# Optimization experiments

Hardware: AMD Instinct MI355X
Metric: run time of the kernel (lower is better)

Reference implementation:

```python
import jax, jax.numpy as jnp
import numpy as np

C = 256
LN_EPS = 1e-5
LEAKY_SLOPE = 0.01

def _layernorm(t, g, b):
    mu = jnp.mean(t, axis=-1, keepdims=True)
    var = jnp.mean((t - mu) ** 2, axis=-1, keepdims=True)
    return (t - mu) * jax.lax.rsqrt(var + LN_EPS) * g + b

def setup_inputs() -> dict:
    key = jax.random.key(0)
    ks = jax.random.split(key, 16)
    b, d, h, w = 4, 4096, 64, 64
    s = lambda n: 1.0 / np.sqrt(n)
    return {
        "x": jax.random.normal(ks[0], (b, 1, d), jnp.float32),
        "y": jax.random.normal(ks[1], (b, C, h, w), jnp.float32),
        "q_w": jax.random.normal(ks[2], (C, C), jnp.float32) * s(C),
        "q_b": jnp.zeros((C,), jnp.float32),
        "dw_w": jax.random.normal(ks[3], (C,), jnp.float32),
        "dw_b": jnp.zeros((C,), jnp.float32),
        "kv_w1": jax.random.normal(ks[4], (1, C // 2), jnp.float32),
        "kv_b1": jnp.zeros((C // 2,), jnp.float32),
        "ln1_g": jnp.ones((C // 2,), jnp.float32),
        "ln1_b": jnp.zeros((C // 2,), jnp.float32),
        "kv_w2": jax.random.normal(ks[5], (C // 2, C), jnp.float32) * s(C // 2),
        "kv_b2": jnp.zeros((C,), jnp.float32),
        "ln2_g": jnp.ones((C,), jnp.float32),
        "ln2_b": jnp.zeros((C,), jnp.float32),
        "kv_w3": jax.random.normal(ks[6], (C, C), jnp.float32) * s(C),
        "kv_b3": jnp.zeros((C,), jnp.float32),
        "ln3_g": jnp.ones((C,), jnp.float32),
        "ln3_b": jnp.zeros((C,), jnp.float32),
        "kv_w4": jax.random.normal(ks[7], (C, 2 * C), jnp.float32) * s(C),
        "kv_b4": jnp.zeros((2 * C,), jnp.float32),
        "proj_w": jax.random.normal(ks[8], (C, C), jnp.float32) * s(C),
        "proj_b": jnp.zeros((C,), jnp.float32),
    }

def reference(x, y, q_w, q_b, dw_w, dw_b, kv_w1, kv_b1, ln1_g, ln1_b,
              kv_w2, kv_b2, ln2_g, ln2_b, kv_w3, kv_b3, ln3_g, ln3_b,
              kv_w4, kv_b4, proj_w, proj_b):
    b, c, h, w = y.shape
    # x: [b, 1, d] -> [b, d, 1]; MLP kv-generator lifts each scalar to 2c channels
    t = jnp.swapaxes(x, 1, 2)  # [b, d, 1]
    t = jax.nn.leaky_relu(_layernorm(t @ kv_w1 + kv_b1, ln1_g, ln1_b), LEAKY_SLOPE)
    t = jax.nn.leaky_relu(_layernorm(t @ kv_w2 + kv_b2, ln2_g, ln2_b), LEAKY_SLOPE)
    t = jax.nn.leaky_relu(_layernorm(t @ kv_w3 + kv_b3, ln3_g, ln3_b), LEAKY_SLOPE)
    t = jax.nn.silu(t @ kv_w4 + kv_b4)  # [b, d, 2c]
    k, v = jnp.split(t, 2, axis=-1)  # each [b, d, c]
    k = jnp.swapaxes(k, 1, 2)  # [b, c, d]
    # q = dwconv1x1(conv1x1(y)): 1x1 conv is a channel matmul; depthwise 1x1 is per-channel affine
    q = jnp.einsum('bchw,oc->bohw', y, q_w) + q_b[None, :, None, None]
    q = q * dw_w[None, :, None, None] + dw_b[None, :, None, None]
    q = q.reshape(b, c, h * w).transpose(0, 2, 1)  # [b, hw, c]
    scores = jnp.einsum('bic,bcd->bid', q, k) * (float(c) ** -0.5)  # [b, hw, d]
    attn = jax.nn.softmax(scores, axis=2)
    h_ = jnp.einsum('bid,bdc->bic', attn, v)  # [b, hw, c]
    h_ = h_.transpose(0, 2, 1).reshape(b, c, h, w)
    h_ = jnp.einsum('bchw,oc->bohw', h_, proj_w) + proj_b[None, :, None, None]
    return y + h_
```

## Files before the change

kernel.cpp:

```cpp
#include <hip/hip_runtime.h>
#include <cstdint>
#include <cstddef>

using bf16   = __bf16;
using bf16x8 = __bf16 __attribute__((ext_vector_type(8)));
using f32x4  = float  __attribute__((ext_vector_type(4)));
using u16    = unsigned short;
using ushort8 = __attribute__((ext_vector_type(8))) unsigned short;

#define MFMA16(a, b, c) __builtin_amdgcn_mfma_f32_16x16x32_bf16(a, b, c, 0, 0, 0)

__device__ __forceinline__ u16 f2bf(float f) {
  union { float f; unsigned u; } v; v.f = f;
  unsigned r = v.u + 0x7fffu + ((v.u >> 16) & 1u);
  return (u16)(r >> 16);
}
__device__ __forceinline__ u16 bfc(float f) {
  union { float f; unsigned u; } v; v.f = f;
  return (u16)((v.u + 0x8000u) >> 16);
}
__device__ __forceinline__ float b2f(u16 h) {
  union { unsigned u; float f; } v; v.u = ((unsigned)h) << 16; return v.f;
}
__device__ __forceinline__ bf16x8 ldb8(const u16* p) { return *(const bf16x8*)p; }
__device__ __forceinline__ float red_sum16(float v) {
  v += __shfl_xor(v, 1, 64); v += __shfl_xor(v, 2, 64);
  v += __shfl_xor(v, 4, 64); v += __shfl_xor(v, 8, 64);
  return v;
}
__device__ __forceinline__ void gll16(const u16* g, u16* l) {
  __builtin_amdgcn_global_load_lds(
      (const __attribute__((address_space(1))) void*)g,
      (__attribute__((address_space(3))) void*)l, 16, 0, 0);
}

#define QSCALE 0.09016844005556021f

__global__ __launch_bounds__(256) void k_prep_mlp1(
    const float* __restrict__ kv_w2, const float* __restrict__ kv_w3,
    const float* __restrict__ kv_w4, const float* __restrict__ q_w,
    const float* __restrict__ proj_w,
    u16* __restrict__ Wt2, u16* __restrict__ Wt3, u16* __restrict__ Wt4,
    u16* __restrict__ Qw, u16* __restrict__ Pww,
    const float* __restrict__ x, const float* __restrict__ w1,
    const float* __restrict__ b1, const float* __restrict__ g, const float* __restrict__ bb,
    u16* __restrict__ T1) {
  if (blockIdx.x >= 4096) {
    int idx = (blockIdx.x - 4096) * 256 + threadIdx.x;
    if (idx < 32768) {
      int n = idx >> 7, k = idx & 127;
      Wt2[idx] = f2bf(kv_w2[k * 256 + n]);
    } else if (idx < 98304) {
      int j = idx - 32768, n = j >> 8, k = j & 255;
      Wt3[j] = f2bf(kv_w3[k * 256 + n]);
    } else if (idx < 229376) {
      int j = idx - 98304, n = j >> 8, k = j & 255;
      Wt4[j] = f2bf(kv_w4[k * 512 + n]);
    } else if (idx < 294912) {
      int j = idx - 229376;
      Qw[j] = f2bf(q_w[j]);
    } else if (idx < 360448) {
      int j = idx - 294912;
      Pww[j] = f2bf(proj_w[j]);
    }
    return;
  }
  int lane = threadIdx.x & 63;
  int r = blockIdx.x * 4 + (threadIdx.x >> 6);
  float xv = x[r];
  float t0 = xv * w1[lane] + b1[lane];
  float t1 = xv * w1[lane + 64] + b1[lane + 64];
  float s = t0 + t1;
  #pragma unroll
  for (int m = 1; m <= 32; m <<= 1) s += __shfl_xor(s, m, 64);
  float mu = s * (1.f / 128.f);
  float d0 = t0 - mu, d1 = t1 - mu;
  float vv = d0 * d0 + d1 * d1;
  #pragma unroll
  for (int m = 1; m <= 32; m <<= 1) vv += __shfl_xor(vv, m, 64);
  float inv = rsqrtf(vv * (1.f / 128.f) + 1e-5f);
  float o0 = d0 * inv * g[lane] + bb[lane];
  float o1 = d1 * inv * g[lane + 64] + bb[lane + 64];
  o0 = o0 > 0.f ? o0 : 0.01f * o0;
  o1 = o1 > 0.f ? o1 : 0.01f * o1;
  T1[(size_t)r * 128 + lane]      = f2bf(o0);
  T1[(size_t)r * 128 + lane + 64] = f2bf(o1);
}

template<int K, int NC>
__global__ __launch_bounds__(128) void k_gemm_ln(const u16* __restrict__ A, const u16* __restrict__ Bt,
    const float* __restrict__ bias, const float* __restrict__ g, const float* __restrict__ bb,
    u16* __restrict__ out) {
  constexpr int LD = K + 8;
  constexpr int CPR = K / 8;
  __shared__ u16 sA[32 * LD];
  __shared__ u16 sB[NC * LD];
  int tid = threadIdx.x, w = tid >> 6, lane = tid & 63, quad = lane >> 4, l16 = lane & 15;
  int i0 = blockIdx.x * 32;
  #pragma unroll
  for (int p = 0; p < (32 * CPR) / 128; ++p) {
    int q = p * 128 + tid; int row = q / CPR, c8 = q - row * CPR;
    *(uint4*)(sA + row * LD + c8 * 8) = *(const uint4*)(A + (size_t)(i0 + row) * K + c8 * 8);
  }
  f32x4 z = {0.f, 0.f, 0.f, 0.f};
  f32x4 acc[16];
  #pragma unroll
  for (int f = 0; f < 16; ++f) acc[f] = z;
  bf16x8 af[K / 32];
  constexpr int NCH = 256 / NC;
  for (int nc = 0; nc < NCH; ++nc) {
    if (nc) __syncthreads();
    #pragma unroll
    for (int p = 0; p < (NC * CPR) / 128; ++p) {
      int q = p * 128 + tid; int row = q / CPR, c8 = q - row * CPR;
      *(uint4*)(sB + row * LD + c8 * 8) = *(const uint4*)(Bt + (size_t)(nc * NC + row) * K + c8 * 8);
    }
    __syncthreads();
    if (nc == 0) {
      #pragma unroll
      for (int kk = 0; kk < K / 32; ++kk) af[kk] = ldb8(sA + (w * 16 + l16) * LD + kk * 32 + quad * 8);
    }
    #pragma unroll
    for (int nb = 0; nb < NC / 16; ++nb) {
      int f = nc * (NC / 16) + nb;
      #pragma unroll
      for (int kk = 0; kk < K / 32; ++kk) {
        bf16x8 bfr = ldb8(sB + (nb * 16 + l16) * LD + kk * 32 + quad * 8);
        acc[f] = MFMA16(af[kk], bfr, acc[f]);
      }
    }
  }
  #pragma unroll
  for (int f = 0; f < 16; ++f) {
    float bv = bias[f * 16 + l16];
    acc[f][0] += bv; acc[f][1] += bv; acc[f][2] += bv; acc[f][3] += bv;
  }
  #pragma unroll
  for (int r = 0; r < 4; ++r) {
    float s = 0;
    #pragma unroll
    for (int f = 0; f < 16; ++f) s += acc[f][r];
    s = red_sum16(s);
    float mu = s * (1.f / 256.f);
    float vv = 0;
    #pragma unroll
    for (int f = 0; f < 16; ++f) { float d = acc[f][r] - mu; vv += d * d; }
    vv = red_sum16(vv);
    float inv = rsqrtf(vv * (1.f / 256.f) + 1e-5f);
    int rowg = i0 + w * 16 + quad * 4 + r;
    #pragma unroll
    for (int f = 0; f < 16; ++f) {
      int col = f * 16 + l16;
      float o = (acc[f][r] - mu) * inv * g[col] + bb[col];
      o = o > 0.f ? o : 0.01f * o;
      out[(size_t)rowg * 256 + col] = f2bf(o);
    }
  }
}

__global__ __launch_bounds__(256) void k_gemm_silu(const u16* __restrict__ A, const u16* __restrict__ Bt,
    const float* __restrict__ bias, u16* __restrict__ Kt, u16* __restrict__ Vt) {
  constexpr int LD = 264, NC = 32;
  __shared__ u16 sA[64 * LD];
  __shared__ u16 sB[NC * LD];
  int tid = threadIdx.x, w = tid >> 6, lane = tid & 63, quad = lane >> 4, l16 = lane & 15;
  int i0 = blockIdx.x * 64;
  int half = blockIdx.y;
  #pragma unroll
  for (int p = 0; p < 8; ++p) {
    int q = p * 256 + tid; int row = q >> 5, c8 = q & 31;
    *(uint4*)(sA + row * LD + c8 * 8) = *(const uint4*)(A + (size_t)(i0 + row) * 256 + c8 * 8);
  }
  f32x4 z = {0.f, 0.f, 0.f, 0.f};
  f32x4 acc[16];
  #pragma unroll
  for (int f = 0; f < 16; ++f) acc[f] = z;
  bf16x8 af[8];
  for (int nc = 0; nc < 8; ++nc) {
    if (nc) __syncthreads();
    #pragma unroll
    for (int p = 0; p < 4; ++p) {
      int q = p * 256 + tid; int row = q >> 5, c8 = q & 31;
      *(uint4*)(sB + row * LD + c8 * 8) =
          *(const uint4*)(Bt + (size_t)(half * 256 + nc * NC + row) * 256 + c8 * 8);
    }
    __syncthreads();
    if (nc == 0) {
      #pragma unroll
      for (int kk = 0; kk < 8; ++kk) af[kk] = ldb8(sA + (w * 16 + l16) * LD + kk * 32 + quad * 8);
    }
    #pragma unroll
    for (int nb = 0; nb < 2; ++nb) {
      int f = nc * 2 + nb;
      #pragma unroll
      for (int kk = 0; kk < 8; ++kk) {
        bf16x8 bfr = ldb8(sB + (nb * 16 + l16) * LD + kk * 32 + quad * 8);
        acc[f] = MFMA16(af[kk], bfr, acc[f]);
      }
    }
  }
  #pragma unroll
  for (int f = 0; f < 16; ++f) {
    int col = f * 16 + l16;
    float bv = bias[half * 256 + col];
    if (half == 0) {
      int chunk = f * 2 + (l16 >> 3), co = col & 7;
      #pragma unroll
      for (int r = 0; r < 4; ++r) {
        int rowg = i0 + w * 16 + quad * 4 + r;
        float v = acc[f][r] + bv;
        v = v / (1.f + __expf(-v));
        int chs = (chunk + (rowg & 31)) & 31;
        Kt[(size_t)rowg * 256 + chs * 8 + co] = f2bf(v);
      }
    } else {
      int rowg0 = i0 + w * 16 + quad * 4;
      int bb2 = rowg0 >> 12, d0 = rowg0 & 4095;
      int dd = d0 & 31, qd = dd >> 3;
      int chs = (qd + (col & 3) + ((col >> 2) & 3)) & 3;
      ushort4 u;
      #pragma unroll
      for (int r = 0; r < 4; ++r) {
        float v = acc[f][r] + bv;
        v = v / (1.f + __expf(-v));
        ((u16*)&u)[r] = f2bf(v);
      }
      size_t off = ((size_t)(bb2 * 128 + (d0 >> 5)) * 8192) + col * 32 + chs * 8 + (dd & 7);
      *(ushort4*)(Vt + off) = u;
    }
  }
}

__global__ __launch_bounds__(128) void k_gemm_q(const float* __restrict__ y, const u16* __restrict__ Qw,
    const float* __restrict__ qb, const float* __restrict__ dww, const float* __restrict__ dwb,
    u16* __restrict__ Qb) {
  __shared__ u16 sY[32 * 72];
  __shared__ u16 sB[256 * 72];
  int tid = threadIdx.x, w = tid >> 6, lane = tid & 63, quad = lane >> 4, l16 = lane & 15;
  int b = blockIdx.x >> 7, i0 = (blockIdx.x & 127) * 32;
  f32x4 z = {0.f, 0.f, 0.f, 0.f};
  f32x4 acc[16];
  #pragma unroll
  for (int f = 0; f < 16; ++f) acc[f] = z;
  for (int kc = 0; kc < 4; ++kc) {
    if (kc) __syncthreads();
    {
      int cl = tid >> 3;
      int il = (tid & 7) * 4;
      #pragma unroll
      for (int p = 0; p < 4; ++p) {
        int c = kc * 64 + p * 16 + cl;
        float4 v = *(const float4*)(y + ((size_t)(b * 256 + c)) * 4096 + i0 + il);
        sY[(il + 0) * 72 + p * 16 + cl] = f2bf(v.x);
        sY[(il + 1) * 72 + p * 16 + cl] = f2bf(v.y);
        sY[(il + 2) * 72 + p * 16 + cl] = f2bf(v.z);
        sY[(il + 3) * 72 + p * 16 + cl] = f2bf(v.w);
      }
    }
    #pragma unroll
    for (int p = 0; p < 16; ++p) {
      int q = p * 128 + tid; int row = q >> 3, k8 = q & 7;
      *(uint4*)(sB + row * 72 + k8 * 8) = *(const uint4*)(Qw + (size_t)row * 256 + kc * 64 + k8 * 8);
    }
    __syncthreads();
    #pragma unroll
    for (int kk = 0; kk < 2; ++kk) {
      bf16x8 af = ldb8(sY + (w * 16 + l16) * 72 + kk * 32 + quad * 8);
      #pragma unroll
      for (int f = 0; f < 16; ++f) {
        bf16x8 bfr = ldb8(sB + (f * 16 + l16) * 72 + kk * 32 + quad * 8);
        acc[f] = MFMA16(af, bfr, acc[f]);
      }
    }
  }
  #pragma unroll
  for (int f = 0; f < 16; ++f) {
    int col = f * 16 + l16;
    float q0 = qb[col], sc = dww[col], dB = dwb[col];
    #pragma unroll
    for (int r = 0; r < 4; ++r) {
      int rowg = i0 + w * 16 + quad * 4 + r;
      float v = ((acc[f][r] + q0) * sc + dB) * QSCALE;
      Qb[((size_t)(b * 4096 + rowg)) * 256 + col] = f2bf(v);
    }
  }
}

__global__ __launch_bounds__(256, 2) void k_attn(const u16* __restrict__ Qb, const u16* __restrict__ Kt,
    const u16* __restrict__ Vt, u16* __restrict__ Op, float* __restrict__ Ol) {
  __shared__ __align__(16) u16 smem[37888];
  int tid = threadIdx.x, w = tid >> 6, lane = tid & 63, quad = lane >> 4, l16 = lane & 15;
  int b = blockIdx.x & 3, kh = (blockIdx.x >> 2) & 3, qt = blockIdx.x >> 4;
  int i0 = qt * 128 + w * 32;

  bf16x8 qf[2][8];
  {
    const u16* qrow = Qb + ((size_t)(b * 4096 + i0 + l16)) * 256 + quad * 8;
    #pragma unroll
    for (int kk = 0; kk < 8; ++kk) {
      qf[0][kk] = ldb8(qrow + kk * 32);
      qf[1][kk] = ldb8(qrow + 16 * 256 + kk * 32);
    }
  }
  f32x4 z = {0.f, 0.f, 0.f, 0.f};
  f32x4 oacc[2][16];
  #pragma unroll
  for (int sub = 0; sub < 2; ++sub)
    #pragma unroll
    for (int f = 0; f < 16; ++f) oacc[sub][f] = z;
  float l4[2][4] = {{0.f, 0.f, 0.f, 0.f}, {0.f, 0.f, 0.f, 0.f}};

  u16* sPw = smem + 32768 + w * 1280;
  int wp = w & 1;
  const u16* gSrc = ((w < 2) ? Kt : Vt) + ((size_t)(b * 128 + kh * 32) * 8192) + wp * 4096 + lane * 8;
  u16* lBase = smem + ((w < 2) ? 0 : 8192) + wp * 4096 + lane * 8;

  #pragma unroll
  for (int i = 0; i < 8; ++i) gll16(gSrc + i * 512, lBase + i * 512);
  gSrc += 8192;

  #pragma unroll 1
  for (int kt = 0; kt < 32; ++kt) {
    int buf = kt & 1;
    const u16* sK = smem + buf * 16384;
    const u16* sV = sK + 8192;
    asm volatile("s_waitcnt vmcnt(0)" ::: "memory");
    __syncthreads();
    if (kt < 31) {
      u16* dst = lBase + (buf ^ 1) * 16384;
      #pragma unroll
      for (int i = 0; i < 8; ++i) gll16(gSrc + i * 512, dst + i * 512);
      gSrc += 8192;
    }
    f32x4 s00 = z, s01 = z, s10 = z, s11 = z;
    #pragma unroll
    for (int kk = 0; kk < 8; ++kk) {
      int ch0 = (kk * 4 + quad + l16) & 31;
      int ch1 = (ch0 + 16) & 31;
      bf16x8 k0 = ldb8(sK + l16 * 256 + ch0 * 8);
      bf16x8 k1 = ldb8(sK + (16 + l16) * 256 + ch1 * 8);
      s00 = MFMA16(qf[0][kk], k0, s00);
      s01 = MFMA16(qf[0][kk], k1, s01);
      s10 = MFMA16(qf[1][kk], k0, s10);
      s11 = MFMA16(qf[1][kk], k1, s11);
    }
    #pragma unroll
    for (int r = 0; r < 4; ++r) {
      float p0 = exp2f(s00[r]);
      float p1 = exp2f(s01[r]);
      float p2 = exp2f(s10[r]);
      float p3 = exp2f(s11[r]);
      l4[0][r] += p0 + p1;
      l4[1][r] += p2 + p3;
      int row0 = (quad * 4 + r) * 40;
      sPw[row0 + l16]            = bfc(p0);
      sPw[row0 + 16 + l16]       = bfc(p1);
      sPw[640 + row0 + l16]      = bfc(p2);
      sPw[640 + row0 + 16 + l16] = bfc(p3);
    }
    asm volatile("s_waitcnt lgkmcnt(0)" ::: "memory");
    bf16x8 pf0 = ldb8(sPw + l16 * 40 + quad * 8);
    bf16x8 pf1 = ldb8(sPw + 640 + l16 * 40 + quad * 8);
    #pragma unroll
    for (int f = 0; f < 16; ++f) {
      int c = f * 16 + l16;
      int chs = (quad + (c & 3) + ((c >> 2) & 3)) & 3;
      bf16x8 vf = ldb8(sV + c * 32 + chs * 8);
      oacc[0][f] = MFMA16(pf0, vf, oacc[0][f]);
      oacc[1][f] = MFMA16(pf1, vf, oacc[1][f]);
    }
  }
  #pragma unroll
  for (int sub = 0; sub < 2; ++sub)
    #pragma unroll
    for (int r = 0; r < 4; ++r) l4[sub][r] = red_sum16(l4[sub][r]);
  #pragma unroll
  for (int sub = 0; sub < 2; ++sub)
    #pragma unroll
    for (int r = 0; r < 4; ++r) {
      size_t gr = (size_t)kh * 16384 + b * 4096 + i0 + sub * 16 + quad * 4 + r;
      u16* orow = Op + gr * 256;
      #pragma unroll
      for (int f = 0; f < 16; ++f) orow[f * 16 + l16] = f2bf(oacc[sub][f][r]);
      if (l16 == 0) Ol[gr] = l4[sub][r];
    }
}

__global__ __launch_bounds__(256) void k_proj(const u16* __restrict__ Op, const float* __restrict__ Ol,
    const u16* __restrict__ Pw, const float* __restrict__ pb, const float* __restrict__ y,
    float* __restrict__ out) {
  __shared__ u16 sA[64 * 136];
  __shared__ u16 sB[64 * 136];
  __shared__ float sW[64];
  int tid = threadIdx.x, w = tid >> 6, lane = tid & 63, quad = lane >> 4, l16 = lane & 15;
  int i0 = blockIdx.x * 64, o0 = blockIdx.y * 64, b = blockIdx.z;
  if (tid < 64) {
    size_t gr = (size_t)b * 4096 + i0 + tid;
    float L = Ol[gr] + Ol[gr + 16384] + Ol[gr + 32768] + Ol[gr + 49152];
    sW[tid] = 1.f / L;
  }
  __syncthreads();
  f32x4 z = {0.f, 0.f, 0.f, 0.f};
  f32x4 acc[4] = {z, z, z, z};
  for (int kc = 0; kc < 2; ++kc) {
    if (kc) __syncthreads();
    #pragma unroll
    for (int p = 0; p < 4; ++p) {
      int q = p * 256 + tid; int row = q >> 4, c8 = q & 15;
      *(uint4*)(sA + row * 136 + c8 * 8) = *(const uint4*)(Pw + ((size_t)(o0 + row)) * 256 + kc * 128 + c8 * 8);
      size_t gr = (size_t)b * 4096 + i0 + row;
      const u16* hp = Op + gr * 256 + kc * 128 + c8 * 8;
      uint4 u0 = *(const uint4*)(hp);
      uint4 u1 = *(const uint4*)(hp + 4194304);
      uint4 u2 = *(const uint4*)(hp + 8388608);
      uint4 u3 = *(const uint4*)(hp + 12582912);
      float wr = sW[row];
      const u16* p0 = (const u16*)&u0; const u16* p1 = (const u16*)&u1;
      const u16* p2 = (const u16*)&u2; const u16* p3 = (const u16*)&u3;
      ushort8 ov;
      #pragma unroll
      for (int e = 0; e < 8; ++e) {
        float v = (b2f(p0[e]) + b2f(p1[e]) + b2f(p2[e]) + b2f(p3[e])) * wr;
        ov[e] = f2bf(v);
      }
      *(ushort8*)(sB + row * 136 + c8 * 8) = ov;
    }
    __syncthreads();
    #pragma unroll
    for (int kk = 0; kk < 4; ++kk) {
      bf16x8 af = ldb8(sA + (w * 16 + l16) * 136 + kk * 32 + quad * 8);
      #pragma unroll
      for (int nb = 0; nb < 4; ++nb) {
        bf16x8 bfr = ldb8(sB + (nb * 16 + l16) * 136 + kk * 32 + quad * 8);
        acc[nb] = MFMA16(af, bfr, acc[nb]);
      }
    }
  }
  #pragma unroll
  for (int nb = 0; nb < 4; ++nb) {
    #pragma unroll
    for (int r = 0; r < 4; ++r) {
      int og = o0 + w * 16 + quad * 4 + r;
      size_t idx = ((size_t)(b * 256 + og)) * 4096 + i0 + nb * 16 + l16;
      out[idx] = y[idx] + acc[nb][r] + pb[og];
    }
  }
}

extern "C" void kernel_launch(void* const* d_in, const int* in_sizes, int n_in,
                              void* d_out, int out_size, void* d_ws, size_t ws_size,
                              hipStream_t stream) {
  (void)in_sizes; (void)n_in; (void)out_size; (void)ws_size;
  const float* x     = (const float*)d_in[0];
  const float* y     = (const float*)d_in[1];
  const float* q_w   = (const float*)d_in[2];
  const float* q_b   = (const float*)d_in[3];
  const float* dw_w  = (const float*)d_in[4];
  const float* dw_b  = (const float*)d_in[5];
  const float* kv_w1 = (const float*)d_in[6];
  const float* kv_b1 = (const float*)d_in[7];
  const float* ln1_g = (const float*)d_in[8];
  const float* ln1_b = (const float*)d_in[9];
  const float* kv_w2 = (const float*)d_in[10];
  const float* kv_b2 = (const float*)d_in[11];
  const float* ln2_g = (const float*)d_in[12];
  const float* ln2_b = (const float*)d_in[13];
  const float* kv_w3 = (const float*)d_in[14];
  const float* kv_b3 = (const float*)d_in[15];
  const float* ln3_g = (const float*)d_in[16];
  const float* ln3_b = (const float*)d_in[17];
  const float* kv_w4 = (const float*)d_in[18];
  const float* kv_b4 = (const float*)d_in[19];
  const float* proj_w = (const float*)d_in[20];
  const float* proj_b = (const float*)d_in[21];
  float* out = (float*)d_out;
  unsigned char* ws = (unsigned char*)d_ws;

  u16* Wt2 = (u16*)(ws + 0);
  u16* Wt3 = (u16*)(ws + 65536);
  u16* Wt4 = (u16*)(ws + 196608);
  u16* Qw  = (u16*)(ws + 458752);
  u16* Pww = (u16*)(ws + 589824);
  u16* T2  = (u16*)(ws + 1048576);
  u16* T3  = (u16*)(ws + 9437184);
  u16* Qb  = T3;
  u16* Kt  = (u16*)(ws + 17825792);
  u16* T1  = Kt;
  u16* Vt  = (u16*)(ws + 26214400);
  u16* Op  = (u16*)(ws + 34603008);
  float* Ol = (float*)(ws + 68157440);

  k_prep_mlp1<<<5504, 256, 0, stream>>>(kv_w2, kv_w3, kv_w4, q_w, proj_w,
                                        Wt2, Wt3, Wt4, Qw, Pww,
                                        x, kv_w1, kv_b1, ln1_g, ln1_b, T1);
  k_gemm_ln<128, 64><<<512, 128, 0, stream>>>(T1, Wt2, kv_b2, ln2_g, ln2_b, T2);
  k_gemm_ln<256, 32><<<512, 128, 0, stream>>>(T2, Wt3, kv_b3, ln3_g, ln3_b, T3);
  k_gemm_silu<<<dim3(256, 2), 256, 0, stream>>>(T3, Wt4, kv_b4, Kt, Vt);
  k_gemm_q<<<512, 128, 0, stream>>>(y, Qw, q_b, dw_w, dw_b, Qb);
  k_attn<<<512, 256, 0, stream>>>(Qb, Kt, Vt, Op, Ol);
  k_proj<<<dim3(64, 4, 4), 256, 0, stream>>>(Op, Ol, Pww, proj_b, y, out);
}
```

Measured before the change: 269.5 us.

## Fuse the kv MLP layers and Q projection into one kernel

The first LayerNorm, the three kv-MLP GEMM+LN layers and the SiLU output layer are merged into one kernel that keeps each 64-row activation tile in shared memory. This removes the intermediate T1/T2/T3 global round trips and several launches. The Q projection runs as extra blocks of the same launch so it can overlap with the MLP blocks. The cost is a larger shared-memory footprint per block and more serialized work per block, with fewer blocks available for the MLP.

Measured after the change: 269.1 us. About the same (-0.1%).

```diff
diff --git a/kernel.cpp b/kernel.cpp
--- a/kernel.cpp
+++ b/kernel.cpp
@@ -36,100 +36,33 @@
 
 #define QSCALE 0.09016844005556021f
 
-__global__ __launch_bounds__(256) void k_prep_mlp1(
-    const float* __restrict__ kv_w2, const float* __restrict__ kv_w3,
-    const float* __restrict__ kv_w4, const float* __restrict__ q_w,
-    const float* __restrict__ proj_w,
-    u16* __restrict__ Wt2, u16* __restrict__ Wt3, u16* __restrict__ Wt4,
-    u16* __restrict__ Qw, u16* __restrict__ Pww,
-    const float* __restrict__ x, const float* __restrict__ w1,
-    const float* __restrict__ b1, const float* __restrict__ g, const float* __restrict__ bb,
-    u16* __restrict__ T1) {
-  if (blockIdx.x >= 4096) {
-    int idx = (blockIdx.x - 4096) * 256 + threadIdx.x;
-    if (idx < 32768) {
-      int n = idx >> 7, k = idx & 127;
-      Wt2[idx] = f2bf(kv_w2[k * 256 + n]);
-    } else if (idx < 98304) {
-      int j = idx - 32768, n = j >> 8, k = j & 255;
-      Wt3[j] = f2bf(kv_w3[k * 256 + n]);
-    } else if (idx < 229376) {
-      int j = idx - 98304, n = j >> 8, k = j & 255;
-      Wt4[j] = f2bf(kv_w4[k * 512 + n]);
-    } else if (idx < 294912) {
-      int j = idx - 229376;
-      Qw[j] = f2bf(q_w[j]);
-    } else if (idx < 360448) {
-      int j = idx - 294912;
-      Pww[j] = f2bf(proj_w[j]);
-    }
-    return;
-  }
-  int lane = threadIdx.x & 63;
-  int r = blockIdx.x * 4 + (threadIdx.x >> 6);
-  float xv = x[r];
-  float t0 = xv * w1[lane] + b1[lane];
-  float t1 = xv * w1[lane + 64] + b1[lane + 64];
-  float s = t0 + t1;
-  #pragma unroll
-  for (int m = 1; m <= 32; m <<= 1) s += __shfl_xor(s, m, 64);
-  float mu = s * (1.f / 128.f);
-  float d0 = t0 - mu, d1 = t1 - mu;
-  float vv = d0 * d0 + d1 * d1;
-  #pragma unroll
-  for (int m = 1; m <= 32; m <<= 1) vv += __shfl_xor(vv, m, 64);
-  float inv = rsqrtf(vv * (1.f / 128.f) + 1e-5f);
-  float o0 = d0 * inv * g[lane] + bb[lane];
-  float o1 = d1 * inv * g[lane + 64] + bb[lane + 64];
-  o0 = o0 > 0.f ? o0 : 0.01f * o0;
-  o1 = o1 > 0.f ? o1 : 0.01f * o1;
-  T1[(size_t)r * 128 + lane]      = f2bf(o0);
-  T1[(size_t)r * 128 + lane + 64] = f2bf(o1);
-}
-
-template<int K, int NC>
-__global__ __launch_bounds__(128) void k_gemm_ln(const u16* __restrict__ A, const u16* __restrict__ Bt,
-    const float* __restrict__ bias, const float* __restrict__ g, const float* __restrict__ bb,
-    u16* __restrict__ out) {
-  constexpr int LD = K + 8;
-  constexpr int CPR = K / 8;
-  __shared__ u16 sA[32 * LD];
-  __shared__ u16 sB[NC * LD];
-  int tid = threadIdx.x, w = tid >> 6, lane = tid & 63, quad = lane >> 4, l16 = lane & 15;
-  int i0 = blockIdx.x * 32;
-  #pragma unroll
-  for (int p = 0; p < (32 * CPR) / 128; ++p) {
-    int q = p * 128 + tid; int row = q / CPR, c8 = q - row * CPR;
-    *(uint4*)(sA + row * LD + c8 * 8) = *(const uint4*)(A + (size_t)(i0 + row) * K + c8 * 8);
-  }
-  f32x4 z = {0.f, 0.f, 0.f, 0.f};
-  f32x4 acc[16];
-  #pragma unroll
-  for (int f = 0; f < 16; ++f) acc[f] = z;
-  bf16x8 af[K / 32];
-  constexpr int NCH = 256 / NC;
-  for (int nc = 0; nc < NCH; ++nc) {
-    if (nc) __syncthreads();
-    #pragma unroll
-    for (int p = 0; p < (NC * CPR) / 128; ++p) {
-      int q = p * 128 + tid; int row = q / CPR, c8 = q - row * CPR;
-      *(uint4*)(sB + row * LD + c8 * 8) = *(const uint4*)(Bt + (size_t)(nc * NC + row) * K + c8 * 8);
-    }
-    __syncthreads();
-    if (nc == 0) {
-      #pragma unroll
-      for (int kk = 0; kk < K / 32; ++kk) af[kk] = ldb8(sA + (w * 16 + l16) * LD + kk * 32 + quad * 8);
-    }
-    #pragma unroll
-    for (int nb = 0; nb < NC / 16; ++nb) {
-      int f = nc * (NC / 16) + nb;
-      #pragma unroll
-      for (int kk = 0; kk < K / 32; ++kk) {
-        bf16x8 bfr = ldb8(sB + (nb * 16 + l16) * LD + kk * 32 + quad * 8);
-        acc[f] = MFMA16(af[kk], bfr, acc[f]);
-      }
-    }
-  }
+__global__ void k_prep(const float* __restrict__ kv_w2, const float* __restrict__ kv_w3,
+                       const float* __restrict__ kv_w4, const float* __restrict__ q_w,
+                       const float* __restrict__ proj_w,
+                       u16* __restrict__ Wt2, u16* __restrict__ Wt3, u16* __restrict__ Wt4,
+                       u16* __restrict__ Qw, u16* __restrict__ Pww) {
+  int idx = blockIdx.x * 256 + threadIdx.x;
+  if (idx < 32768) {
+    int n = idx >> 7, k = idx & 127;
+    Wt2[idx] = f2bf(kv_w2[k * 256 + n]);
+  } else if (idx < 98304) {
+    int j = idx - 32768, n = j >> 8, k = j & 255;
+    Wt3[j] = f2bf(kv_w3[k * 256 + n]);
+  } else if (idx < 229376) {
+    int j = idx - 98304, n = j >> 8, k = j & 255;
+    Wt4[j] = f2bf(kv_w4[k * 512 + n]);
+  } else if (idx < 294912) {
+    int j = idx - 229376;
+    Qw[j] = f2bf(q_w[j]);
+  } else if (idx < 360448) {
+    int j = idx - 294912;
+    Pww[j] = f2bf(proj_w[j]);
+  }
+}
+
+__device__ __forceinline__ void ln_store(f32x4* acc, const float* __restrict__ bias,
+    const float* __restrict__ g, const float* __restrict__ bb, u16* act,
+    int w, int quad, int l16) {
   #pragma unroll
   for (int f = 0; f < 16; ++f) {
     float bv = bias[f * 16 + l16];
@@ -147,97 +80,166 @@
     for (int f = 0; f < 16; ++f) { float d = acc[f][r] - mu; vv += d * d; }
     vv = red_sum16(vv);
     float inv = rsqrtf(vv * (1.f / 256.f) + 1e-5f);
-    int rowg = i0 + w * 16 + quad * 4 + r;
+    int rl = w * 16 + quad * 4 + r;
     #pragma unroll
     for (int f = 0; f < 16; ++f) {
       int col = f * 16 + l16;
       float o = (acc[f][r] - mu) * inv * g[col] + bb[col];
       o = o > 0.f ? o : 0.01f * o;
-      out[(size_t)rowg * 256 + col] = f2bf(o);
-    }
-  }
-}
-
-__global__ __launch_bounds__(256) void k_gemm_silu(const u16* __restrict__ A, const u16* __restrict__ Bt,
-    const float* __restrict__ bias, u16* __restrict__ Kt, u16* __restrict__ Vt) {
-  constexpr int LD = 264, NC = 32;
-  __shared__ u16 sA[64 * LD];
-  __shared__ u16 sB[NC * LD];
-  int tid = threadIdx.x, w = tid >> 6, lane = tid & 63, quad = lane >> 4, l16 = lane & 15;
-  int i0 = blockIdx.x * 64;
-  int half = blockIdx.y;
-  #pragma unroll
-  for (int p = 0; p < 8; ++p) {
-    int q = p * 256 + tid; int row = q >> 5, c8 = q & 31;
-    *(uint4*)(sA + row * LD + c8 * 8) = *(const uint4*)(A + (size_t)(i0 + row) * 256 + c8 * 8);
-  }
+      act[rl * 264 + col] = f2bf(o);
+    }
+  }
+}
+
+template<int K>
+__device__ __forceinline__ void mlp_layer(u16* act, u16* sW, const u16* __restrict__ Wt,
+    const float* __restrict__ bias, const float* __restrict__ g, const float* __restrict__ bb,
+    int tid, int w, int quad, int l16) {
+  bf16x8 af[K / 32];
+  #pragma unroll
+  for (int kk = 0; kk < K / 32; ++kk) af[kk] = ldb8(act + (w * 16 + l16) * 264 + kk * 32 + quad * 8);
   f32x4 z = {0.f, 0.f, 0.f, 0.f};
   f32x4 acc[16];
   #pragma unroll
   for (int f = 0; f < 16; ++f) acc[f] = z;
-  bf16x8 af[8];
   for (int nc = 0; nc < 8; ++nc) {
-    if (nc) __syncthreads();
-    #pragma unroll
-    for (int p = 0; p < 4; ++p) {
-      int q = p * 256 + tid; int row = q >> 5, c8 = q & 31;
-      *(uint4*)(sB + row * LD + c8 * 8) =
-          *(const uint4*)(Bt + (size_t)(half * 256 + nc * NC + row) * 256 + c8 * 8);
-    }
     __syncthreads();
-    if (nc == 0) {
-      #pragma unroll
-      for (int kk = 0; kk < 8; ++kk) af[kk] = ldb8(sA + (w * 16 + l16) * LD + kk * 32 + quad * 8);
-    }
+    #pragma unroll
+    for (int p = 0; p < K / 64; ++p) {
+      int q = p * 256 + tid; int row = q / (K / 8), c8 = q % (K / 8);
+      *(uint4*)(sW + row * 264 + c8 * 8) = *(const uint4*)(Wt + (size_t)(nc * 32 + row) * K + c8 * 8);
+    }
+    __syncthreads();
     #pragma unroll
     for (int nb = 0; nb < 2; ++nb) {
       int f = nc * 2 + nb;
       #pragma unroll
-      for (int kk = 0; kk < 8; ++kk) {
-        bf16x8 bfr = ldb8(sB + (nb * 16 + l16) * LD + kk * 32 + quad * 8);
-        acc[f] = MFMA16(af[kk], bfr, acc[f]);
-      }
-    }
-  }
-  #pragma unroll
-  for (int f = 0; f < 16; ++f) {
-    int col = f * 16 + l16;
-    float bv = bias[half * 256 + col];
-    if (half == 0) {
-      int chunk = f * 2 + (l16 >> 3), co = col & 7;
-      #pragma unroll
-      for (int r = 0; r < 4; ++r) {
-        int rowg = i0 + w * 16 + quad * 4 + r;
-        float v = acc[f][r] + bv;
-        v = v / (1.f + __expf(-v));
-        int chs = (chunk + (rowg & 31)) & 31;
-        Kt[(size_t)rowg * 256 + chs * 8 + co] = f2bf(v);
-      }
-    } else {
-      int rowg0 = i0 + w * 16 + quad * 4;
-      int bb2 = rowg0 >> 12, d0 = rowg0 & 4095;
-      int dd = d0 & 31, qd = dd >> 3;
-      int chs = (qd + (col & 3) + ((col >> 2) & 3)) & 3;
-      ushort4 u;
-      #pragma unroll
-      for (int r = 0; r < 4; ++r) {
-        float v = acc[f][r] + bv;
-        v = v / (1.f + __expf(-v));
-        ((u16*)&u)[r] = f2bf(v);
-      }
-      size_t off = ((size_t)(bb2 * 128 + (d0 >> 5)) * 8192) + col * 32 + chs * 8 + (dd & 7);
-      *(ushort4*)(Vt + off) = u;
-    }
-  }
-}
-
-__global__ __launch_bounds__(128) void k_gemm_q(const float* __restrict__ y, const u16* __restrict__ Qw,
+      for (int kk = 0; kk < K / 32; ++kk)
+        acc[f] = MFMA16(af[kk], ldb8(sW + (nb * 16 + l16) * 264 + kk * 32 + quad * 8), acc[f]);
+    }
+  }
+  ln_store(acc, bias, g, bb, act, w, quad, l16);
+  __syncthreads();
+}
+
+__device__ __forceinline__ void mlp_layer4(u16* act, u16* sW, const u16* __restrict__ Wt4,
+    const float* __restrict__ bias4, u16* __restrict__ Kt, u16* __restrict__ Vt,
+    int i0, int tid, int w, int quad, int l16) {
+  bf16x8 af[8];
+  #pragma unroll
+  for (int kk = 0; kk < 8; ++kk) af[kk] = ldb8(act + (w * 16 + l16) * 264 + kk * 32 + quad * 8);
+  f32x4 z = {0.f, 0.f, 0.f, 0.f};
+  for (int h = 0; h < 2; ++h) {
+    f32x4 acc[16];
+    #pragma unroll
+    for (int f = 0; f < 16; ++f) acc[f] = z;
+    for (int nc = 0; nc < 8; ++nc) {
+      __syncthreads();
+      #pragma unroll
+      for (int p = 0; p < 4; ++p) {
+        int q = p * 256 + tid; int row = q >> 5, c8 = q & 31;
+        *(uint4*)(sW + row * 264 + c8 * 8) =
+            *(const uint4*)(Wt4 + (size_t)(h * 256 + nc * 32 + row) * 256 + c8 * 8);
+      }
+      __syncthreads();
+      #pragma unroll
+      for (int nb = 0; nb < 2; ++nb) {
+        int f = nc * 2 + nb;
+        #pragma unroll
+        for (int kk = 0; kk < 8; ++kk)
+          acc[f] = MFMA16(af[kk], ldb8(sW + (nb * 16 + l16) * 264 + kk * 32 + quad * 8), acc[f]);
+      }
+    }
+    #pragma unroll
+    for (int f = 0; f < 16; ++f) {
+      int col = f * 16 + l16;
+      float bv = bias4[h * 256 + col];
+      if (h == 0) {
+        int chunk = f * 2 + (l16 >> 3), co = col & 7;
+        #pragma unroll
+        for (int r = 0; r < 4; ++r) {
+          int rowg = i0 + w * 16 + quad * 4 + r;
+          float v = acc[f][r] + bv;
+          v = v / (1.f + __expf(-v));
+          int chs = (chunk + (rowg & 31)) & 31;
+          Kt[(size_t)rowg * 256 + chs * 8 + co] = f2bf(v);
+        }
+      } else {
+        int rowg0 = i0 + w * 16 + quad * 4;
+        int bb2 = rowg0 >> 12, d0 = rowg0 & 4095;
+        int dd = d0 & 31, qd = dd >> 3;
+        int chs = (qd + (col & 3) + ((col >> 2) & 3)) & 3;
+        ushort4 u;
+        #pragma unroll
+        for (int r = 0; r < 4; ++r) {
+          float v = acc[f][r] + bv;
+          v = v / (1.f + __expf(-v));
+          ((u16*)&u)[r] = f2bf(v);
+        }
+        size_t off = ((size_t)(bb2 * 128 + (d0 >> 5)) * 8192) + col * 32 + chs * 8 + (dd & 7);
+        *(ushort4*)(Vt + off) = u;
+      }
+    }
+  }
+}
+
+__global__ __launch_bounds__(256, 2) void k_fused(
+    const float* __restrict__ x, const float* __restrict__ w1, const float* __restrict__ bias1,
+    const float* __restrict__ g1, const float* __restrict__ bb1,
+    const u16* __restrict__ Wt2, const float* __restrict__ bias2,
+    const float* __restrict__ g2, const float* __restrict__ bb2,
+    const u16* __restrict__ Wt3, const float* __restrict__ bias3,
+    const float* __restrict__ g3, const float* __restrict__ bb3,
+    const u16* __restrict__ Wt4, const float* __restrict__ bias4,
+    const float* __restrict__ y, const u16* __restrict__ Qw,
     const float* __restrict__ qb, const float* __restrict__ dww, const float* __restrict__ dwb,
-    u16* __restrict__ Qb) {
-  __shared__ u16 sY[32 * 72];
-  __shared__ u16 sB[256 * 72];
+    u16* __restrict__ Kt, u16* __restrict__ Vt, u16* __restrict__ Qb) {
+  __shared__ __align__(16) u16 smem[25344];
   int tid = threadIdx.x, w = tid >> 6, lane = tid & 63, quad = lane >> 4, l16 = lane & 15;
-  int b = blockIdx.x >> 7, i0 = (blockIdx.x & 127) * 32;
+
+  if (blockIdx.x < 256) {
+    u16* act = smem;
+    u16* sW  = smem + 16896;
+    int i0 = blockIdx.x * 64;
+    {
+      int rloc = w * 16 + (lane >> 2);
+      int c0 = (lane & 3) * 32;
+      float xv = x[i0 + rloc];
+      float t[32];
+      float s = 0.f;
+      #pragma unroll
+      for (int j = 0; j < 32; ++j) { t[j] = xv * w1[c0 + j] + bias1[c0 + j]; s += t[j]; }
+      s += __shfl_xor(s, 1, 64); s += __shfl_xor(s, 2, 64);
+      float mu = s * (1.f / 128.f);
+      float vv = 0.f;
+      #pragma unroll
+      for (int j = 0; j < 32; ++j) { float d = t[j] - mu; vv += d * d; }
+      vv += __shfl_xor(vv, 1, 64); vv += __shfl_xor(vv, 2, 64);
+      float inv = rsqrtf(vv * (1.f / 128.f) + 1e-5f);
+      #pragma unroll
+      for (int jo = 0; jo < 4; ++jo) {
+        ushort8 pk;
+        #pragma unroll
+        for (int e = 0; e < 8; ++e) {
+          int j = jo * 8 + e;
+          float o = (t[j] - mu) * inv * g1[c0 + j] + bb1[c0 + j];
+          o = o > 0.f ? o : 0.01f * o;
+          pk[e] = f2bf(o);
+        }
+        *(ushort8*)(act + rloc * 264 + c0 + jo * 8) = pk;
+      }
+    }
+    __syncthreads();
+    mlp_layer<128>(act, sW, Wt2, bias2, g2, bb2, tid, w, quad, l16);
+    mlp_layer<256>(act, sW, Wt3, bias3, g3, bb3, tid, w, quad, l16);
+    mlp_layer4(act, sW, Wt4, bias4, Kt, Vt, i0, tid, w, quad, l16);
+    return;
+  }
+
+  u16* sY = smem;
+  u16* sB = smem + 4608;
+  int t = blockIdx.x - 256;
+  int b = t >> 6, i0 = (t & 63) * 64;
   f32x4 z = {0.f, 0.f, 0.f, 0.f};
   f32x4 acc[16];
   #pragma unroll
@@ -245,8 +247,8 @@
   for (int kc = 0; kc < 4; ++kc) {
     if (kc) __syncthreads();
     {
-      int cl = tid >> 3;
-      int il = (tid & 7) * 4;
+      int cl = tid >> 4;
+      int il = (tid & 15) * 4;
       #pragma unroll
       for (int p = 0; p < 4; ++p) {
         int c = kc * 64 + p * 16 + cl;
@@ -258,8 +260,8 @@
       }
     }
     #pragma unroll
-    for (int p = 0; p < 16; ++p) {
-      int q = p * 128 + tid; int row = q >> 3, k8 = q & 7;
+    for (int p = 0; p < 8; ++p) {
+      int q = p * 256 + tid; int row = q >> 3, k8 = q & 7;
       *(uint4*)(sB + row * 72 + k8 * 8) = *(const uint4*)(Qw + (size_t)row * 256 + kc * 64 + k8 * 8);
     }
     __syncthreads();
@@ -481,22 +483,19 @@
   u16* Wt4 = (u16*)(ws + 196608);
   u16* Qw  = (u16*)(ws + 458752);
   u16* Pww = (u16*)(ws + 589824);
-  u16* T2  = (u16*)(ws + 1048576);
-  u16* T3  = (u16*)(ws + 9437184);
-  u16* Qb  = T3;
+  u16* Qb  = (u16*)(ws + 9437184);
   u16* Kt  = (u16*)(ws + 17825792);
-  u16* T1  = Kt;
   u16* Vt  = (u16*)(ws + 26214400);
   u16* Op  = (u16*)(ws + 34603008);
   float* Ol = (float*)(ws + 68157440);
 
-  k_prep_mlp1<<<5504, 256, 0, stream>>>(kv_w2, kv_w3, kv_w4, q_w, proj_w,
-                                        Wt2, Wt3, Wt4, Qw, Pww,
-                                        x, kv_w1, kv_b1, ln1_g, ln1_b, T1);
-  k_gemm_ln<128, 64><<<512, 128, 0, stream>>>(T1, Wt2, kv_b2, ln2_g, ln2_b, T2);
-  k_gemm_ln<256, 32><<<512, 128, 0, stream>>>(T2, Wt3, kv_b3, ln3_g, ln3_b, T3);
-  k_gemm_silu<<<dim3(256, 2), 256, 0, stream>>>(T3, Wt4, kv_b4, Kt, Vt);
-  k_gemm_q<<<512, 128, 0, stream>>>(y, Qw, q_b, dw_w, dw_b, Qb);
+  k_prep<<<1408, 256, 0, stream>>>(kv_w2, kv_w3, kv_w4, q_w, proj_w, Wt2, Wt3, Wt4, Qw, Pww);
+  k_fused<<<512, 256, 0, stream>>>(x, kv_w1, kv_b1, ln1_g, ln1_b,
+                                   Wt2, kv_b2, ln2_g, ln2_b,
+                                   Wt3, kv_b3, ln3_g, ln3_b,
+                                   Wt4, kv_b4,
+                                   y, Qw, q_b, dw_w, dw_b,
+                                   Kt, Vt, Qb);
   k_attn<<<512, 256, 0, stream>>>(Qb, Kt, Vt, Op, Ol);
   k_proj<<<dim3(64, 4, 4), 256, 0, stream>>>(Op, Ol, Pww, proj_b, y, out);
 }
```
